# Optimization experiments

Measured on AMD Instinct MI355X. Metric: run time of the kernel, lower is better.

Reference implementation:

```python
import jax, jax.numpy as jnp
import numpy as np

T, D, N, K, H, F = 2048, 4096, 32, 8, 128, 14336
THETA = 500000.0
EPS = 1e-5


def setup_inputs() -> dict:
    key = jax.random.key(0)
    ks = jax.random.split(key, 10)
    s = 0.02  # weight init scale
    return {
        "x": jax.random.normal(ks[0], (T, D), jnp.float32),
        "positions": jnp.arange(T, dtype=jnp.int32),
        "ln1_scale": jnp.ones((D,), jnp.float32),
        "w_q": jax.random.normal(ks[1], (D, N, H), jnp.float32) * s,
        "w_k": jax.random.normal(ks[2], (D, K, H), jnp.float32) * s,
        "w_v": jax.random.normal(ks[3], (D, K, H), jnp.float32) * s,
        "w_o": jax.random.normal(ks[4], (N, H, D), jnp.float32) * s,
        "ln2_scale": jnp.ones((D,), jnp.float32),
        "w_gate": jax.random.normal(ks[5], (D, F), jnp.float32) * s,
        "w_up": jax.random.normal(ks[6], (D, F), jnp.float32) * s,
        "w_down": jax.random.normal(ks[7], (F, D), jnp.float32) * s,
    }


def _rms_norm(x, scale):
    var = jnp.mean(jnp.square(x), axis=-1, keepdims=True)
    return x * jax.lax.rsqrt(var + EPS) * scale


def _apply_rope(x, pos):
    # x: [T, heads, H]; Llama rotate-half RoPE
    half = H // 2
    inv_freq = 1.0 / (THETA ** (jnp.arange(half, dtype=jnp.float32) / half))
    ang = pos.astype(jnp.float32)[:, None] * inv_freq[None, :]      # [T, half]
    cos = jnp.cos(ang)[:, None, :]
    sin = jnp.sin(ang)[:, None, :]
    x1, x2 = x[..., :half], x[..., half:]
    return jnp.concatenate([x1 * cos - x2 * sin, x2 * cos + x1 * sin], axis=-1)


def reference(x, positions, ln1_scale, w_q, w_k, w_v, w_o, ln2_scale, w_gate, w_up, w_down):
    # --- input RMSNorm ---
    h = _rms_norm(x, ln1_scale)
    # --- QKV projections + RoPE ---
    q = _apply_rope(jnp.einsum('td,dnh->tnh', h, w_q), positions)   # [T,N,H]
    k = _apply_rope(jnp.einsum('td,dkh->tkh', h, w_k), positions)   # [T,K,H]
    v = jnp.einsum('td,dkh->tkh', h, w_v)                            # [T,K,H]
    # --- GQA causal attention (prefill) ---
    G = N // K
    qg = q.reshape(T, K, G, H)
    scale = 1.0 / jnp.sqrt(jnp.float32(H))
    scores = jnp.einsum('tkgh,skh->kgts', qg, k) * scale             # [K,G,T,T]
    causal = positions[:, None] >= positions[None, :]                # [T,T]
    scores = jnp.where(causal[None, None], scores, jnp.finfo(scores.dtype).min)
    probs = jax.nn.softmax(scores, axis=-1)
    attn = jnp.einsum('kgts,skh->tkgh', probs, v).reshape(T, N, H)
    attn_out = jnp.einsum('tnh,nhd->td', attn, w_o)
    # --- residual ---
    residual = attn_out + x
    # --- post-attn RMSNorm + SwiGLU MLP ---
    h2 = _rms_norm(residual, ln2_scale)
    gate = jax.nn.silu(h2 @ w_gate)
    up = h2 @ w_up
    out = (gate * up) @ w_down
    return residual + out
```

## Files before the change

kernel.cpp:

```cpp
#include <hip/hip_runtime.h>

typedef __attribute__((ext_vector_type(8))) short bf16x8;
typedef __attribute__((ext_vector_type(4))) float f32x4;

constexpr int T = 2048;
constexpr int D = 4096;
constexpr int NQ = 32;
constexpr int NKV = 8;
constexpr int H = 128;
constexpr int F = 14336;
constexpr int NQKV = (NQ + 2 * NKV) * H;
constexpr int VOFF = (NQ + NKV) * H;

__device__ inline unsigned short f2bf(float f) {
  unsigned u = __float_as_uint(f);
  return (unsigned short)((u + 0x7FFFu + ((u >> 16) & 1u)) >> 16);
}

__device__ inline void gload_lds16(const void* g, void* l) {
  __builtin_amdgcn_global_load_lds((const __attribute__((address_space(1))) void*)g,
                                   (__attribute__((address_space(3))) void*)l, 16, 0, 0);
}

#define MFMA16(a, b, c) __builtin_amdgcn_mfma_f32_16x16x32_bf16(a, b, c, 0, 0, 0)

template <int MODE>
__global__ __launch_bounds__(256) void transpose_bf16(const float* __restrict__ in,
                                                      unsigned short* __restrict__ out,
                                                      int K, int N) {
  __shared__ float tile[64 * 65];
  const int kb = blockIdx.x * 64;
  const int nb = blockIdx.y * 64;
  const int tid = threadIdx.x;
  const int r = tid >> 2;
  const int c4 = tid & 3;
#pragma unroll
  for (int i = 0; i < 4; ++i) {
    float4 v = *(const float4*)(in + (size_t)(kb + r) * N + nb + c4 * 16 + i * 4);
    *(float4*)&tile[r * 65 + c4 * 16 + i * 4] = v;
  }
  __syncthreads();
  const int n = tid >> 2;
  const int kq = tid & 3;
  int nsrc = nb + n;
  int prow = (MODE == 0) ? nsrc : ((nsrc >> 4) * 32 + (nsrc & 15) + (MODE == 2 ? 16 : 0));
#pragma unroll
  for (int half = 0; half < 2; ++half) {
    ushort4 o0, o1;
    int k0 = kq * 16 + half * 8;
    o0.x = f2bf(tile[(k0 + 0) * 65 + n]);
    o0.y = f2bf(tile[(k0 + 1) * 65 + n]);
    o0.z = f2bf(tile[(k0 + 2) * 65 + n]);
    o0.w = f2bf(tile[(k0 + 3) * 65 + n]);
    o1.x = f2bf(tile[(k0 + 4) * 65 + n]);
    o1.y = f2bf(tile[(k0 + 5) * 65 + n]);
    o1.z = f2bf(tile[(k0 + 6) * 65 + n]);
    o1.w = f2bf(tile[(k0 + 7) * 65 + n]);
    unsigned short* op = out + (size_t)prow * K + kb + k0;
    *(ushort4*)(op + 0) = o0;
    *(ushort4*)(op + 4) = o1;
  }
}

__global__ __launch_bounds__(256) void rmsnorm_kernel(
    const float* __restrict__ in, const float* __restrict__ scale,
    unsigned short* __restrict__ out) {
  int row = blockIdx.x;
  const float4* xr = (const float4*)(in + (size_t)row * D);
  const float4* sr = (const float4*)scale;
  float4 vals[4];
  float ss = 0.f;
#pragma unroll
  for (int i = 0; i < 4; ++i) {
    float4 v = xr[threadIdx.x + i * 256];
    vals[i] = v;
    ss += v.x * v.x + v.y * v.y + v.z * v.z + v.w * v.w;
  }
#pragma unroll
  for (int off = 32; off; off >>= 1) ss += __shfl_xor(ss, off, 64);
  __shared__ float wsum[4];
  if ((threadIdx.x & 63) == 0) wsum[threadIdx.x >> 6] = ss;
  __syncthreads();
  float r = rsqrtf((wsum[0] + wsum[1] + wsum[2] + wsum[3]) * (1.f / D) + 1e-5f);
#pragma unroll
  for (int i = 0; i < 4; ++i) {
    int vi = threadIdx.x + i * 256;
    float4 v = vals[i];
    float4 s = sr[vi];
    ushort4 o;
    o.x = f2bf(v.x * r * s.x);
    o.y = f2bf(v.y * r * s.y);
    o.z = f2bf(v.z * r * s.z);
    o.w = f2bf(v.w * r * s.w);
    *(ushort4*)(out + (size_t)row * D + (size_t)vi * 4) = o;
  }
}

__global__ __launch_bounds__(256) void add3_kernel(const float* __restrict__ a,
                                                   const float* __restrict__ b,
                                                   const float* __restrict__ c,
                                                   float* __restrict__ o) {
  int i = blockIdx.x * 256 + threadIdx.x;
  float4 va = ((const float4*)a)[i];
  float4 vb = ((const float4*)b)[i];
  float4 vc = ((const float4*)c)[i];
  float4 vo;
  vo.x = va.x + vb.x + vc.x;
  vo.y = va.y + vb.y + vc.y;
  vo.z = va.z + vb.z + vc.z;
  vo.w = va.w + vb.w + vc.w;
  ((float4*)o)[i] = vo;
}

__global__ __launch_bounds__(256) void rope_table(const int* __restrict__ pos,
                                                  float* __restrict__ ctab,
                                                  float* __restrict__ stab) {
  int idx = blockIdx.x * 256 + threadIdx.x;
  int t = idx >> 6, i = idx & 63;
  float inv = exp2f(-(float)i * (log2f(500000.0f) / 64.0f));
  float ang = (float)pos[t] * inv;
  ctab[idx] = cosf(ang);
  stab[idx] = sinf(ang);
}

__global__ __launch_bounds__(256) void rope_bf16(const float* __restrict__ x,
                                                 const float* __restrict__ ctab,
                                                 const float* __restrict__ stab,
                                                 unsigned short* __restrict__ out,
                                                 int nheads, int row_stride, float scale) {
  int idx = blockIdx.x * 256 + threadIdx.x;
  int i = idx & 63;
  int tn = idx >> 6;
  int t = tn / nheads;
  int n = tn - t * nheads;
  float c = ctab[t * 64 + i], s = stab[t * 64 + i];
  const float* p = x + (size_t)t * row_stride + n * H;
  float x1 = p[i], x2 = p[i + 64];
  unsigned short* o = out + (size_t)tn * H;
  o[i] = f2bf((x1 * c - x2 * s) * scale);
  o[i + 64] = f2bf((x2 * c + x1 * s) * scale);
}

template <int EP>
__global__ __launch_bounds__(256) void gemm_bf(
    const unsigned short* __restrict__ A, const unsigned short* __restrict__ Bt0,
    float* __restrict__ outF, unsigned short* __restrict__ outB, int Kd, int Nd) {
  __shared__ unsigned short lA[128 * 32];
  __shared__ unsigned short lB0[128 * 32];

  const int tid = threadIdx.x;
  const int m0 = blockIdx.x * 128;
  const int n0 = blockIdx.y * 128;
  const int lane = tid & 63;
  const int wv = tid >> 6;

  f32x4 acc[4][4];
#pragma unroll
  for (int i = 0; i < 4; ++i)
#pragma unroll
    for (int j = 0; j < 4; ++j) acc[i][j] = (f32x4){0.f, 0.f, 0.f, 0.f};

  const int wr = (wv >> 1) * 64;
  const int wc = (wv & 1) * 64;
  const int k8 = (lane >> 4) * 8;
  const int rl = lane & 15;
  const int sidx0 = wv * 512 + lane * 8;

  for (int k0 = 0; k0 < Kd; k0 += 32) {
    __syncthreads();
#pragma unroll
    for (int it = 0; it < 2; ++it) {
      int idx = sidx0 + it * 2048;
      int row = idx >> 5, kk = idx & 31;
      int base = wv * 512 + it * 2048;
      gload_lds16(A + (size_t)(m0 + row) * Kd + k0 + kk, &lA[base]);
      gload_lds16(Bt0 + (size_t)(n0 + row) * Kd + k0 + kk, &lB0[base]);
    }
    asm volatile("s_waitcnt vmcnt(0)" ::: "memory");
    __syncthreads();

    bf16x8 af[4], bfr[4];
#pragma unroll
    for (int i = 0; i < 4; ++i)
      af[i] = *(const bf16x8*)&lA[(wr + i * 16 + rl) * 32 + k8];
#pragma unroll
    for (int j = 0; j < 4; ++j)
      bfr[j] = *(const bf16x8*)&lB0[(wc + j * 16 + rl) * 32 + k8];
#pragma unroll
    for (int i = 0; i < 4; ++i)
#pragma unroll
      for (int j = 0; j < 4; ++j)
        acc[i][j] = MFMA16(af[i], bfr[j], acc[i][j]);
  }

  const int rb = (lane >> 4) * 4;
#pragma unroll
  for (int i = 0; i < 4; ++i)
#pragma unroll
    for (int j = 0; j < 4; ++j) {
      int col = n0 + wc + j * 16 + rl;
      if (EP == 4 && n0 >= VOFF) {
        int row0 = m0 + wr + i * 16 + rb;
        ushort4 o;
        o.x = f2bf(acc[i][j][0]);
        o.y = f2bf(acc[i][j][1]);
        o.z = f2bf(acc[i][j][2]);
        o.w = f2bf(acc[i][j][3]);
        *(ushort4*)&outB[(size_t)(col - VOFF) * T + row0] = o;
      } else {
#pragma unroll
        for (int jj = 0; jj < 4; ++jj) {
          int row = m0 + wr + i * 16 + rb + jj;
          outF[(size_t)row * Nd + col] = acc[i][j][jj];
        }
      }
    }
}

template <int EP>
__global__ __launch_bounds__(512, 2) void gemm256(
    const unsigned short* __restrict__ A, const unsigned short* __restrict__ Bt,
    float* __restrict__ outF, float* __restrict__ outF2,
    unsigned short* __restrict__ outB, int Kd, int Nd, int Klen) {
  __shared__ unsigned short lds[65536];
  const int tid = threadIdx.x, lane = tid & 63, wv = tid >> 6;
  const int wm = wv >> 2, wn = wv & 3;
  const int rl = lane & 15, g = lane >> 4;
  const int kz = blockIdx.z;
  int raw = blockIdx.x + blockIdx.y * gridDim.x;
  int cpx = (gridDim.x * gridDim.y) >> 3;
  int sid = (raw & 7) * cpx + (raw >> 3);
  int brow = sid % gridDim.x;
  int bcol = sid / gridDim.x;
  const int m0 = brow * 256, n0 = bcol * 256;

  const int l8 = lane >> 3;
  const int scol = ((lane & 7) ^ l8) * 8;
  const int xr = (rl & 7) << 4;
  const int pc0 = (g * 16) ^ xr;
  const int pc1 = (64 + g * 16) ^ xr;

  const char* ldsc = (const char*)lds;
  const unsigned short* gA = A + (size_t)(m0 + wv * 8 + l8) * Kd + kz * Klen + scol;
  const unsigned short* gB = Bt + (size_t)(n0 + wv * 8 + l8) * Kd + kz * Klen + scol;

  f32x4 acc[8][4];
#pragma unroll
  for (int i = 0; i < 8; ++i)
#pragma unroll
    for (int j = 0; j < 4; ++j) acc[i][j] = (f32x4){0.f, 0.f, 0.f, 0.f};

  const int NT = Klen >> 6;

#define STAGE_A(kt)                                                              \
  {                                                                              \
    int b_ = (kt) & 1;                                                           \
    const unsigned short* s_ = gA + (size_t)(kt) * 64;                           \
    gload_lds16(s_, (void*)&lds[b_ * 32768 + wv * 512]);                         \
    gload_lds16(s_ + (size_t)64 * Kd, (void*)&lds[b_ * 32768 + (8 + wv) * 512]); \
    gload_lds16(s_ + (size_t)128 * Kd, (void*)&lds[b_ * 32768 + 8192 + wv * 512]); \
    gload_lds16(s_ + (size_t)192 * Kd,                                           \
                (void*)&lds[b_ * 32768 + 8192 + (8 + wv) * 512]);                \
  }
#define STAGE_B(kt)                                                              \
  {                                                                              \
    int b_ = (kt) & 1;                                                           \
    const unsigned short* s_ = gB + (size_t)(kt) * 64;                           \
    gload_lds16(s_, (void*)&lds[b_ * 32768 + 16384 + wv * 512]);                 \
    gload_lds16(s_ + (size_t)64 * Kd,                                            \
                (void*)&lds[b_ * 32768 + 16384 + (8 + wv) * 512]);               \
    gload_lds16(s_ + (size_t)128 * Kd,                                           \
                (void*)&lds[b_ * 32768 + 24576 + wv * 512]);                     \
    gload_lds16(s_ + (size_t)192 * Kd,                                           \
                (void*)&lds[b_ * 32768 + 24576 + (8 + wv) * 512]);               \
  }
#define SBAR()                        \
  __builtin_amdgcn_sched_barrier(0);  \
  __builtin_amdgcn_s_barrier();

  STAGE_A(0); STAGE_B(0);
  STAGE_B(1); STAGE_A(1);
  asm volatile("s_waitcnt vmcnt(8)" ::: "memory");
  SBAR();

  const int bhalf = (wn >> 1) * 16384;
  const int brl = (wn & 1) * 64;
  bf16x8 b0c[2][2];
  {
    const char* bB0 = ldsc + 32768 + bhalf;
#pragma unroll
    for (int nf = 0; nf < 2; ++nf) {
      b0c[nf][0] = *(const bf16x8*)(bB0 + (brl + nf * 16 + rl) * 128 + pc0);
      b0c[nf][1] = *(const bf16x8*)(bB0 + (brl + nf * 16 + rl) * 128 + pc1);
    }
  }

  for (int kt = 0; kt < NT; ++kt) {
    const int b = kt & 1;
    const char* aB = ldsc + b * 65536 + wm * 16384;
    const char* bB = ldsc + b * 65536 + 32768 + bhalf;
    const char* bBn = ldsc + (b ^ 1) * 65536 + 32768 + bhalf;
    bf16x8 aR[4][2], bR1[2][2], b0n[2][2];
#pragma unroll
    for (int mf = 0; mf < 4; ++mf) {
      aR[mf][0] = *(const bf16x8*)(aB + (mf * 16 + rl) * 128 + pc0);
      aR[mf][1] = *(const bf16x8*)(aB + (mf * 16 + rl) * 128 + pc1);
    }
    SBAR();
    __builtin_amdgcn_s_setprio(1);
#pragma unroll
    for (int mf = 0; mf < 4; ++mf)
#pragma unroll
      for (int nf = 0; nf < 2; ++nf) {
        acc[mf][nf] = MFMA16(aR[mf][0], b0c[nf][0], acc[mf][nf]);
        acc[mf][nf] = MFMA16(aR[mf][1], b0c[nf][1], acc[mf][nf]);
      }
    __builtin_amdgcn_s_setprio(0);
    SBAR();
#pragma unroll
    for (int nf = 0; nf < 2; ++nf) {
      bR1[nf][0] = *(const bf16x8*)(bB + (brl + (nf + 2) * 16 + rl) * 128 + pc0);
      bR1[nf][1] = *(const bf16x8*)(bB + (brl + (nf + 2) * 16 + rl) * 128 + pc1);
    }
    SBAR();
    __builtin_amdgcn_s_setprio(1);
#pragma unroll
    for (int mf = 0; mf < 4; ++mf)
#pragma unroll
      for (int nf = 0; nf < 2; ++nf) {
        acc[mf][nf + 2] = MFMA16(aR[mf][0], bR1[nf][0], acc[mf][nf + 2]);
        acc[mf][nf + 2] = MFMA16(aR[mf][1], bR1[nf][1], acc[mf][nf + 2]);
      }
    __builtin_amdgcn_s_setprio(0);
    SBAR();
    if (kt + 2 < NT) STAGE_B(kt + 2);
#pragma unroll
    for (int mf = 0; mf < 4; ++mf) {
      aR[mf][0] = *(const bf16x8*)(aB + ((mf + 4) * 16 + rl) * 128 + pc0);
      aR[mf][1] = *(const bf16x8*)(aB + ((mf + 4) * 16 + rl) * 128 + pc1);
    }
    if (kt + 2 < NT) {
      asm volatile("s_waitcnt vmcnt(8)" ::: "memory");
    } else if (kt + 1 < NT) {
      asm volatile("s_waitcnt vmcnt(4)" ::: "memory");
    }
    SBAR();
    __builtin_amdgcn_s_setprio(1);
#pragma unroll
    for (int mf = 0; mf < 4; ++mf)
#pragma unroll
      for (int nf = 0; nf < 2; ++nf) {
        acc[mf + 4][nf + 2] = MFMA16(aR[mf][0], bR1[nf][0], acc[mf + 4][nf + 2]);
        acc[mf + 4][nf + 2] = MFMA16(aR[mf][1], bR1[nf][1], acc[mf + 4][nf + 2]);
      }
    __builtin_amdgcn_s_setprio(0);
    SBAR();
    if (kt + 2 < NT) STAGE_A(kt + 2);
#pragma unroll
    for (int nf = 0; nf < 2; ++nf) {
      b0n[nf][0] = *(const bf16x8*)(bBn + (brl + nf * 16 + rl) * 128 + pc0);
      b0n[nf][1] = *(const bf16x8*)(bBn + (brl + nf * 16 + rl) * 128 + pc1);
    }
    SBAR();
    __builtin_amdgcn_s_setprio(1);
#pragma unroll
    for (int mf = 0; mf < 4; ++mf)
#pragma unroll
      for (int nf = 0; nf < 2; ++nf) {
        acc[mf + 4][nf] = MFMA16(aR[mf][0], b0c[nf][0], acc[mf + 4][nf]);
        acc[mf + 4][nf] = MFMA16(aR[mf][1], b0c[nf][1], acc[mf + 4][nf]);
      }
    __builtin_amdgcn_s_setprio(0);
    if (kt + 2 < NT) {
      asm volatile("s_waitcnt vmcnt(8)" ::: "memory");
    } else if (kt + 1 < NT) {
      asm volatile("s_waitcnt vmcnt(0)" ::: "memory");
    }
    SBAR();
#pragma unroll
    for (int nf = 0; nf < 2; ++nf) {
      b0c[nf][0] = b0n[nf][0];
      b0c[nf][1] = b0n[nf][1];
    }
  }

  const int g4 = g * 4;
  if constexpr (EP == 5) {
    const int acolBase = ((n0 + wn * 64) >> 1) + rl;
#pragma unroll
    for (int mf = 0; mf < 8; ++mf)
#pragma unroll
      for (int p = 0; p < 2; ++p) {
        int acol = acolBase + p * 16;
#pragma unroll
        for (int jj = 0; jj < 4; ++jj) {
          int row = m0 + wm * 128 + mf * 16 + g4 + jj;
          float gg = acc[mf][2 * p][jj];
          float uu = acc[mf][2 * p + 1][jj];
          outB[(size_t)row * F + acol] = f2bf(gg / (1.f + __expf(-gg)) * uu);
        }
      }
  } else {
    float* dst = kz ? outF2 : outF;
#pragma unroll
    for (int mf = 0; mf < 8; ++mf)
#pragma unroll
      for (int q = 0; q < 4; ++q) {
        int col = n0 + wn * 64 + q * 16 + rl;
#pragma unroll
        for (int jj = 0; jj < 4; ++jj) {
          int row = m0 + wm * 128 + mf * 16 + g4 + jj;
          dst[(size_t)row * Nd + col] = acc[mf][q][jj];
        }
      }
  }
#undef STAGE_A
#undef STAGE_B
#undef SBAR
}

constexpr int KLD = 136;
constexpr int VLD = 72;
constexpr int PLD = 72;

__global__ __launch_bounds__(256) void flash_attn(
    const unsigned short* __restrict__ qbf, const unsigned short* __restrict__ kbf,
    const unsigned short* __restrict__ vtbf, unsigned short* __restrict__ out) {
  __shared__ unsigned short K_lds[64 * KLD];
  __shared__ unsigned short Vt_lds[H * VLD];
  __shared__ unsigned short P_lds[4 * 16 * PLD];

  const int tid = threadIdx.x;
  const int lane = tid & 63;
  const int wave = tid >> 6;
  const int qb = blockIdx.x;
  const int n = blockIdx.y;
  const int kvh = n >> 2;
  const int g = lane >> 4;
  const int rl = lane & 15;
  const int qrow = qb * 64 + wave * 16;

  bf16x8 qfrag[4];
  {
    const unsigned short* qp = qbf + ((size_t)(qrow + rl) * NQ + n) * H + g * 8;
#pragma unroll
    for (int ks = 0; ks < 4; ++ks) qfrag[ks] = *(const bf16x8*)(qp + ks * 32);
  }

  f32x4 oacc[8];
#pragma unroll
  for (int ob = 0; ob < 8; ++ob) oacc[ob] = (f32x4){0.f, 0.f, 0.f, 0.f};
  float mrun[4] = {-1e30f, -1e30f, -1e30f, -1e30f};
  float lrun[4] = {0.f, 0.f, 0.f, 0.f};

  const int krow = tid >> 2, kseg = (tid & 3) * 32;
  const int vh = tid >> 1, vseg = (tid & 1) * 32;

  for (int kt = 0; kt <= qb; ++kt) {
    const int kbase = kt * 64;
    __syncthreads();
    {
      const unsigned short* kp = kbf + ((size_t)(kbase + krow) * NKV + kvh) * H + kseg;
#pragma unroll
      for (int i = 0; i < 4; ++i)
        *(bf16x8*)&K_lds[krow * KLD + kseg + i * 8] = *(const bf16x8*)(kp + i * 8);
      const unsigned short* vp = vtbf + (size_t)(kvh * H + vh) * T + kbase + vseg;
#pragma unroll
      for (int i = 0; i < 4; ++i)
        *(bf16x8*)&Vt_lds[vh * VLD + vseg + i * 8] = *(const bf16x8*)(vp + i * 8);
    }
    __syncthreads();

    f32x4 sacc[4];
#pragma unroll
    for (int cb = 0; cb < 4; ++cb) sacc[cb] = (f32x4){0.f, 0.f, 0.f, 0.f};
#pragma unroll
    for (int cb = 0; cb < 4; ++cb)
#pragma unroll
      for (int ks = 0; ks < 4; ++ks) {
        bf16x8 kf = *(const bf16x8*)&K_lds[(cb * 16 + rl) * KLD + ks * 32 + g * 8];
        sacc[cb] = MFMA16(qfrag[ks], kf, sacc[cb]);
      }

    if (kt == qb) {
#pragma unroll
      for (int cb = 0; cb < 4; ++cb) {
        int kvg = cb * 16 + rl;
#pragma unroll
        for (int r = 0; r < 4; ++r) {
          int qrel = wave * 16 + g * 4 + r;
          if (kvg > qrel) sacc[cb][r] = -1e30f;
        }
      }
    }

    float mx[4], sm[4], corr[4];
#pragma unroll
    for (int r = 0; r < 4; ++r) {
      float m0 = fmaxf(fmaxf(sacc[0][r], sacc[1][r]), fmaxf(sacc[2][r], sacc[3][r]));
#pragma unroll
      for (int off = 1; off < 16; off <<= 1) m0 = fmaxf(m0, __shfl_xor(m0, off, 64));
      float nm = fmaxf(mrun[r], m0);
      corr[r] = __expf(mrun[r] - nm);
      mrun[r] = nm;
      mx[r] = nm;
    }
#pragma unroll
    for (int cb = 0; cb < 4; ++cb)
#pragma unroll
      for (int r = 0; r < 4; ++r) sacc[cb][r] = __expf(sacc[cb][r] - mx[r]);
#pragma unroll
    for (int r = 0; r < 4; ++r) {
      float s0 = sacc[0][r] + sacc[1][r] + sacc[2][r] + sacc[3][r];
#pragma unroll
      for (int off = 1; off < 16; off <<= 1) s0 += __shfl_xor(s0, off, 64);
      sm[r] = s0;
      lrun[r] = lrun[r] * corr[r] + sm[r];
    }
#pragma unroll
    for (int ob = 0; ob < 8; ++ob)
#pragma unroll
      for (int r = 0; r < 4; ++r) oacc[ob][r] *= corr[r];

#pragma unroll
    for (int cb = 0; cb < 4; ++cb)
#pragma unroll
      for (int r = 0; r < 4; ++r)
        P_lds[(wave * 16 + g * 4 + r) * PLD + cb * 16 + rl] = f2bf(sacc[cb][r]);

    bf16x8 pa[2];
#pragma unroll
    for (int ks = 0; ks < 2; ++ks)
      pa[ks] = *(const bf16x8*)&P_lds[(wave * 16 + rl) * PLD + ks * 32 + g * 8];

#pragma unroll
    for (int ob = 0; ob < 8; ++ob)
#pragma unroll
      for (int ks = 0; ks < 2; ++ks) {
        bf16x8 vf = *(const bf16x8*)&Vt_lds[(ob * 16 + rl) * VLD + ks * 32 + g * 8];
        oacc[ob] = MFMA16(pa[ks], vf, oacc[ob]);
      }
  }

  float inv[4];
#pragma unroll
  for (int r = 0; r < 4; ++r) inv[r] = 1.f / lrun[r];
#pragma unroll
  for (int ob = 0; ob < 8; ++ob)
#pragma unroll
    for (int r = 0; r < 4; ++r) {
      int t = qrow + g * 4 + r;
      out[((size_t)t * NQ + n) * H + ob * 16 + rl] = f2bf(oacc[ob][r] * inv[r]);
    }
}

extern "C" void kernel_launch(void* const* d_in, const int* in_sizes, int n_in,
                              void* d_out, int out_size, void* d_ws, size_t ws_size,
                              hipStream_t stream) {
  (void)in_sizes; (void)n_in; (void)out_size; (void)ws_size;
  const float* x = (const float*)d_in[0];
  const int* positions = (const int*)d_in[1];
  const float* ln1 = (const float*)d_in[2];
  const float* w_q = (const float*)d_in[3];
  const float* w_k = (const float*)d_in[4];
  const float* w_v = (const float*)d_in[5];
  const float* w_o = (const float*)d_in[6];
  const float* ln2 = (const float*)d_in[7];
  const float* w_gate = (const float*)d_in[8];
  const float* w_up = (const float*)d_in[9];
  const float* w_down = (const float*)d_in[10];
  float* out = (float*)d_out;

  char* ws = (char*)d_ws;
  size_t off = 0;
  auto alloc = [&](size_t bytes) {
    char* p = ws + off;
    off += (bytes + 255) & ~(size_t)255;
    return p;
  };
  unsigned short* h_bf = (unsigned short*)alloc((size_t)T * D * 2);
  unsigned short* h2_bf = (unsigned short*)alloc((size_t)T * D * 2);
  unsigned short* attn_bf = (unsigned short*)alloc((size_t)T * NQ * H * 2);
  unsigned short* act_bf = (unsigned short*)alloc((size_t)T * F * 2);
  float* qkvf = (float*)alloc((size_t)T * NQKV * 4);
  float* resid = (float*)alloc((size_t)T * D * 4);
  float* ctab = (float*)alloc((size_t)T * 64 * 4);
  float* stab = (float*)alloc((size_t)T * 64 * 4);
  unsigned short* qbf = (unsigned short*)alloc((size_t)T * NQ * H * 2);
  unsigned short* kbf = (unsigned short*)alloc((size_t)T * NKV * H * 2);
  unsigned short* vtbf = (unsigned short*)alloc((size_t)NKV * H * T * 2);
  unsigned short* wqkvt = (unsigned short*)alloc((size_t)NQKV * D * 2);
  unsigned short* wot = (unsigned short*)alloc((size_t)D * NQ * H * 2);
  unsigned short* wgut = (unsigned short*)alloc((size_t)2 * F * D * 2);
  unsigned short* wdt = (unsigned short*)alloc((size_t)D * F * 2);
  float* part0 = qkvf;
  float* part1 = (float*)wqkvt;

  transpose_bf16<0><<<dim3(D / 64, (NQ * H) / 64), 256, 0, stream>>>(w_q, wqkvt, D, NQ * H);
  transpose_bf16<0><<<dim3(D / 64, (NKV * H) / 64), 256, 0, stream>>>(
      w_k, wqkvt + (size_t)NQ * H * D, D, NKV * H);
  transpose_bf16<0><<<dim3(D / 64, (NKV * H) / 64), 256, 0, stream>>>(
      w_v, wqkvt + (size_t)VOFF * D, D, NKV * H);
  transpose_bf16<0><<<dim3((NQ * H) / 64, D / 64), 256, 0, stream>>>(w_o, wot, NQ * H, D);
  transpose_bf16<1><<<dim3(D / 64, F / 64), 256, 0, stream>>>(w_gate, wgut, D, F);
  transpose_bf16<2><<<dim3(D / 64, F / 64), 256, 0, stream>>>(w_up, wgut, D, F);
  transpose_bf16<0><<<dim3(F / 64, D / 64), 256, 0, stream>>>(w_down, wdt, F, D);

  rmsnorm_kernel<<<T, 256, 0, stream>>>(x, ln1, h_bf);
  rope_table<<<(T * 64) / 256, 256, 0, stream>>>(positions, ctab, stab);
  gemm_bf<4><<<dim3(T / 128, NQKV / 128), 256, 0, stream>>>(
      h_bf, wqkvt, qkvf, vtbf, D, NQKV);
  rope_bf16<<<(T * NQ * 64) / 256, 256, 0, stream>>>(qkvf, ctab, stab, qbf, NQ, NQKV,
                                                     0.08838834764831845f);
  rope_bf16<<<(T * NKV * 64) / 256, 256, 0, stream>>>(qkvf + NQ * H, ctab, stab, kbf,
                                                      NKV, NQKV, 1.0f);
  flash_attn<<<dim3(T / 64, NQ), 256, 0, stream>>>(qbf, kbf, vtbf, attn_bf);
  gemm256<0><<<dim3(T / 256, D / 256, 2), 512, 0, stream>>>(
      attn_bf, wot, part0, part1, nullptr, NQ * H, D, NQ * H / 2);
  add3_kernel<<<(T * D / 4) / 256, 256, 0, stream>>>(part0, part1, x, resid);
  rmsnorm_kernel<<<T, 256, 0, stream>>>(resid, ln2, h2_bf);
  gemm256<5><<<dim3(T / 256, (2 * F) / 256), 512, 0, stream>>>(
      h2_bf, wgut, nullptr, nullptr, act_bf, D, 2 * F, D);
  gemm256<0><<<dim3(T / 256, D / 256, 2), 512, 0, stream>>>(
      act_bf, wdt, part0, part1, nullptr, F, D, F / 2);
  add3_kernel<<<(T * D / 4) / 256, 256, 0, stream>>>(part0, part1, resid, out);
}
```

Before: 1.459 ms.

## Spread GEMM global-to-LDS prefetch across MFMA phases and drop cross-buffer B carry

The main bf16 GEMM loop no longer preloads the next tile's B fragment from the other LDS buffer, and no longer carries it in registers across iterations. Each iteration now reads its own B-low fragment at the top. The global-to-LDS staging of tile kt+2 is split into per-quarter loads placed between the MFMA phases, and one barrier plus a mid-loop vmcnt wait are removed. The goal is to smooth memory traffic and cut barrier and wait overhead. The trade-off is exposed LDS read latency at the start of each iteration and a changed order of outstanding loads against the fixed vmcnt(8) wait.

Result: faster. 1.401 ms (-4.0%).

```diff
diff --git a/kernel.cpp b/kernel.cpp
--- a/kernel.cpp
+++ b/kernel.cpp
@@ -252,59 +252,41 @@
 
   const int NT = Klen >> 6;
 
-#define STAGE_A(kt)                                                              \
-  {                                                                              \
-    int b_ = (kt) & 1;                                                           \
-    const unsigned short* s_ = gA + (size_t)(kt) * 64;                           \
-    gload_lds16(s_, (void*)&lds[b_ * 32768 + wv * 512]);                         \
-    gload_lds16(s_ + (size_t)64 * Kd, (void*)&lds[b_ * 32768 + (8 + wv) * 512]); \
-    gload_lds16(s_ + (size_t)128 * Kd, (void*)&lds[b_ * 32768 + 8192 + wv * 512]); \
-    gload_lds16(s_ + (size_t)192 * Kd,                                           \
-                (void*)&lds[b_ * 32768 + 8192 + (8 + wv) * 512]);                \
-  }
-#define STAGE_B(kt)                                                              \
-  {                                                                              \
-    int b_ = (kt) & 1;                                                           \
-    const unsigned short* s_ = gB + (size_t)(kt) * 64;                           \
-    gload_lds16(s_, (void*)&lds[b_ * 32768 + 16384 + wv * 512]);                 \
-    gload_lds16(s_ + (size_t)64 * Kd,                                            \
-                (void*)&lds[b_ * 32768 + 16384 + (8 + wv) * 512]);               \
-    gload_lds16(s_ + (size_t)128 * Kd,                                           \
-                (void*)&lds[b_ * 32768 + 24576 + wv * 512]);                     \
-    gload_lds16(s_ + (size_t)192 * Kd,                                           \
-                (void*)&lds[b_ * 32768 + 24576 + (8 + wv) * 512]);               \
-  }
+#define STAGE_AL(kt, l)                                                      \
+  gload_lds16(gA + (size_t)(kt) * 64 + (size_t)(l) * 64 * Kd,                \
+              (void*)&lds[((kt) & 1) * 32768 + (l) * 4096 + wv * 512]);
+#define STAGE_BL(kt, l)                                                      \
+  gload_lds16(gB + (size_t)(kt) * 64 + (size_t)(l) * 64 * Kd,                \
+              (void*)&lds[((kt) & 1) * 32768 + 16384 + (l) * 4096 + wv * 512]);
 #define SBAR()                        \
   __builtin_amdgcn_sched_barrier(0);  \
   __builtin_amdgcn_s_barrier();
 
-  STAGE_A(0); STAGE_B(0);
-  STAGE_B(1); STAGE_A(1);
+  STAGE_AL(0, 0); STAGE_AL(0, 1); STAGE_AL(0, 2); STAGE_AL(0, 3);
+  STAGE_BL(0, 0); STAGE_BL(0, 1); STAGE_BL(0, 2); STAGE_BL(0, 3);
+  STAGE_AL(1, 0); STAGE_AL(1, 1); STAGE_AL(1, 2); STAGE_AL(1, 3);
+  STAGE_BL(1, 0); STAGE_BL(1, 1); STAGE_BL(1, 2); STAGE_BL(1, 3);
   asm volatile("s_waitcnt vmcnt(8)" ::: "memory");
   SBAR();
 
   const int bhalf = (wn >> 1) * 16384;
   const int brl = (wn & 1) * 64;
-  bf16x8 b0c[2][2];
-  {
-    const char* bB0 = ldsc + 32768 + bhalf;
-#pragma unroll
-    for (int nf = 0; nf < 2; ++nf) {
-      b0c[nf][0] = *(const bf16x8*)(bB0 + (brl + nf * 16 + rl) * 128 + pc0);
-      b0c[nf][1] = *(const bf16x8*)(bB0 + (brl + nf * 16 + rl) * 128 + pc1);
-    }
-  }
 
   for (int kt = 0; kt < NT; ++kt) {
     const int b = kt & 1;
     const char* aB = ldsc + b * 65536 + wm * 16384;
     const char* bB = ldsc + b * 65536 + 32768 + bhalf;
-    const char* bBn = ldsc + (b ^ 1) * 65536 + 32768 + bhalf;
-    bf16x8 aR[4][2], bR1[2][2], b0n[2][2];
+    const bool pre = (kt + 2 < NT);
+    bf16x8 aLo[4][2], aHi[4][2], bLo[2][2], bHi[2][2];
 #pragma unroll
     for (int mf = 0; mf < 4; ++mf) {
-      aR[mf][0] = *(const bf16x8*)(aB + (mf * 16 + rl) * 128 + pc0);
-      aR[mf][1] = *(const bf16x8*)(aB + (mf * 16 + rl) * 128 + pc1);
+      aLo[mf][0] = *(const bf16x8*)(aB + (mf * 16 + rl) * 128 + pc0);
+      aLo[mf][1] = *(const bf16x8*)(aB + (mf * 16 + rl) * 128 + pc1);
+    }
+#pragma unroll
+    for (int nf = 0; nf < 2; ++nf) {
+      bLo[nf][0] = *(const bf16x8*)(bB + (brl + nf * 16 + rl) * 128 + pc0);
+      bLo[nf][1] = *(const bf16x8*)(bB + (brl + nf * 16 + rl) * 128 + pc1);
     }
     SBAR();
     __builtin_amdgcn_s_setprio(1);
@@ -312,76 +294,64 @@
     for (int mf = 0; mf < 4; ++mf)
 #pragma unroll
       for (int nf = 0; nf < 2; ++nf) {
-        acc[mf][nf] = MFMA16(aR[mf][0], b0c[nf][0], acc[mf][nf]);
-        acc[mf][nf] = MFMA16(aR[mf][1], b0c[nf][1], acc[mf][nf]);
+        acc[mf][nf] = MFMA16(aLo[mf][0], bLo[nf][0], acc[mf][nf]);
+        acc[mf][nf] = MFMA16(aLo[mf][1], bLo[nf][1], acc[mf][nf]);
       }
     __builtin_amdgcn_s_setprio(0);
     SBAR();
 #pragma unroll
     for (int nf = 0; nf < 2; ++nf) {
-      bR1[nf][0] = *(const bf16x8*)(bB + (brl + (nf + 2) * 16 + rl) * 128 + pc0);
-      bR1[nf][1] = *(const bf16x8*)(bB + (brl + (nf + 2) * 16 + rl) * 128 + pc1);
-    }
+      bHi[nf][0] = *(const bf16x8*)(bB + (brl + (nf + 2) * 16 + rl) * 128 + pc0);
+      bHi[nf][1] = *(const bf16x8*)(bB + (brl + (nf + 2) * 16 + rl) * 128 + pc1);
+    }
+    if (pre) { STAGE_AL(kt + 2, 0); STAGE_AL(kt + 2, 2); }
     SBAR();
     __builtin_amdgcn_s_setprio(1);
 #pragma unroll
     for (int mf = 0; mf < 4; ++mf)
 #pragma unroll
       for (int nf = 0; nf < 2; ++nf) {
-        acc[mf][nf + 2] = MFMA16(aR[mf][0], bR1[nf][0], acc[mf][nf + 2]);
-        acc[mf][nf + 2] = MFMA16(aR[mf][1], bR1[nf][1], acc[mf][nf + 2]);
+        acc[mf][nf + 2] = MFMA16(aLo[mf][0], bHi[nf][0], acc[mf][nf + 2]);
+        acc[mf][nf + 2] = MFMA16(aLo[mf][1], bHi[nf][1], acc[mf][nf + 2]);
       }
     __builtin_amdgcn_s_setprio(0);
     SBAR();
-    if (kt + 2 < NT) STAGE_B(kt + 2);
 #pragma unroll
     for (int mf = 0; mf < 4; ++mf) {
-      aR[mf][0] = *(const bf16x8*)(aB + ((mf + 4) * 16 + rl) * 128 + pc0);
-      aR[mf][1] = *(const bf16x8*)(aB + ((mf + 4) * 16 + rl) * 128 + pc1);
-    }
-    if (kt + 2 < NT) {
-      asm volatile("s_waitcnt vmcnt(8)" ::: "memory");
-    } else if (kt + 1 < NT) {
-      asm volatile("s_waitcnt vmcnt(4)" ::: "memory");
-    }
+      aHi[mf][0] = *(const bf16x8*)(aB + ((mf + 4) * 16 + rl) * 128 + pc0);
+      aHi[mf][1] = *(const bf16x8*)(aB + ((mf + 4) * 16 + rl) * 128 + pc1);
+    }
+    if (pre) { STAGE_BL(kt + 2, 0); STAGE_BL(kt + 2, 1); }
     SBAR();
     __builtin_amdgcn_s_setprio(1);
 #pragma unroll
     for (int mf = 0; mf < 4; ++mf)
 #pragma unroll
       for (int nf = 0; nf < 2; ++nf) {
-        acc[mf + 4][nf + 2] = MFMA16(aR[mf][0], bR1[nf][0], acc[mf + 4][nf + 2]);
-        acc[mf + 4][nf + 2] = MFMA16(aR[mf][1], bR1[nf][1], acc[mf + 4][nf + 2]);
+        acc[mf + 4][nf + 2] = MFMA16(aHi[mf][0], bHi[nf][0], acc[mf + 4][nf + 2]);
+        acc[mf + 4][nf + 2] = MFMA16(aHi[mf][1], bHi[nf][1], acc[mf + 4][nf + 2]);
       }
     __builtin_amdgcn_s_setprio(0);
     SBAR();
-    if (kt + 2 < NT) STAGE_A(kt + 2);
-#pragma unroll
-    for (int nf = 0; nf < 2; ++nf) {
-      b0n[nf][0] = *(const bf16x8*)(bBn + (brl + nf * 16 + rl) * 128 + pc0);
-      b0n[nf][1] = *(const bf16x8*)(bBn + (brl + nf * 16 + rl) * 128 + pc1);
-    }
-    SBAR();
+    if (pre) {
+      STAGE_BL(kt + 2, 2); STAGE_BL(kt + 2, 3);
+      STAGE_AL(kt + 2, 1); STAGE_AL(kt + 2, 3);
+    }
     __builtin_amdgcn_s_setprio(1);
 #pragma unroll
     for (int mf = 0; mf < 4; ++mf)
 #pragma unroll
       for (int nf = 0; nf < 2; ++nf) {
-        acc[mf + 4][nf] = MFMA16(aR[mf][0], b0c[nf][0], acc[mf + 4][nf]);
-        acc[mf + 4][nf] = MFMA16(aR[mf][1], b0c[nf][1], acc[mf + 4][nf]);
+        acc[mf + 4][nf] = MFMA16(aHi[mf][0], bLo[nf][0], acc[mf + 4][nf]);
+        acc[mf + 4][nf] = MFMA16(aHi[mf][1], bLo[nf][1], acc[mf + 4][nf]);
       }
     __builtin_amdgcn_s_setprio(0);
-    if (kt + 2 < NT) {
+    if (pre) {
       asm volatile("s_waitcnt vmcnt(8)" ::: "memory");
     } else if (kt + 1 < NT) {
       asm volatile("s_waitcnt vmcnt(0)" ::: "memory");
     }
     SBAR();
-#pragma unroll
-    for (int nf = 0; nf < 2; ++nf) {
-      b0c[nf][0] = b0n[nf][0];
-      b0c[nf][1] = b0n[nf][1];
-    }
   }
 
   const int g4 = g * 4;
@@ -414,8 +384,8 @@
         }
       }
   }
-#undef STAGE_A
-#undef STAGE_B
+#undef STAGE_AL
+#undef STAGE_BL
 #undef SBAR
 }
 
```
